# Kernel tuning notes

Measured on AMD Instinct MI355X. Metric: run time of the kernel, lower is better.

Reference implementation:

```python
import jax, jax.numpy as jnp
from jax import lax
import numpy as np

B, S, D, H = 16, 4096, 256, 256


def setup_inputs() -> dict:
    key = jax.random.key(0)
    k1, k2, k3, k4 = jax.random.split(key, 4)
    scale_x = 1.0 / np.sqrt(D)
    scale_h = 1.0 / np.sqrt(H)
    return {
        "inputs": jax.random.normal(k1, (B, S, D), dtype=jnp.float32),
        "state0": jnp.zeros((B, H), dtype=jnp.float32),
        "Wx": jax.random.normal(k2, (D, H), dtype=jnp.float32) * scale_x,
        "Wh": jax.random.normal(k3, (H, H), dtype=jnp.float32) * scale_h,
        "b": jnp.zeros((H,), dtype=jnp.float32),
    }


def reference(inputs, state0, Wx, Wh, b):
    # inputs: [B, S, D] -> time-major [S, B, D] (mirrors inputs.transpose_(0,1))
    x_tm = jnp.transpose(inputs, (1, 0, 2))
    # Precompute the input projection for all timesteps in one GEMM
    x_proj = jnp.einsum("sbd,dh->sbh", x_tm, Wx) + b  # [S, B, H]

    def step(h, xp_t):
        h_new = jnp.tanh(xp_t + h @ Wh)  # cell update; get_output = identity
        return h_new, h_new  # dropout p=0.0 -> identity

    _, outs = lax.scan(step, state0, x_proj)  # outs: [S, B, H]
    return jnp.transpose(outs, (1, 0, 2))  # back to [B, S, H]
```

## Files before the change

kernel.cpp:

```cpp
#include <hip/hip_runtime.h>

#define B_ 16
#define S_ 4096
#define D_ 256
#define H_ 256

typedef _Float16 h2 __attribute__((ext_vector_type(2)));
typedef _Float16 h8 __attribute__((ext_vector_type(8)));
typedef float f4 __attribute__((ext_vector_type(4)));

static __device__ __forceinline__ float fdot2f(h2 a, h2 b, float c) {
    return __builtin_amdgcn_fdot2(a, b, c, false);
}

template <int CTRL>
static __device__ __forceinline__ float dpp_qp(float v) {
    int r = __builtin_amdgcn_update_dpp(0, __float_as_int(v), CTRL, 0xF, 0xF, true);
    return __int_as_float(r);
}
#define DPP_XOR1 0xB1
#define DPP_XOR2 0x4E

static __device__ __forceinline__ int swz(int i) {
    const int s = i >> 6, r = (i >> 3) & 7, e = i & 7;
    return 64 * s + 8 * ((r + 2 * s) & 7) + e;
}

__global__ __launch_bounds__(256) void xproj_kernel(
    const float* __restrict__ x, const float* __restrict__ Wx,
    const float* __restrict__ bias, float* __restrict__ out)
{
    __shared__ float xs[32 * 256];
    const int tid = threadIdx.x;
    const long long row0 = (long long)blockIdx.x * 32;

    {
        const f4* __restrict__ xg = (const f4*)(x + row0 * D_);
        f4* xsv = (f4*)xs;
        #pragma unroll
        for (int k = 0; k < 8; ++k)
            xsv[tid + k * 256] = xg[tid + k * 256];
    }
    __syncthreads();

    const int j = tid;
    float acc[32];
    const float bj = bias[j];
    #pragma unroll
    for (int r = 0; r < 32; ++r) acc[r] = bj;

    for (int d4 = 0; d4 < D_ / 4; ++d4) {
        const float w0 = Wx[(d4 * 4 + 0) * H_ + j];
        const float w1 = Wx[(d4 * 4 + 1) * H_ + j];
        const float w2 = Wx[(d4 * 4 + 2) * H_ + j];
        const float w3 = Wx[(d4 * 4 + 3) * H_ + j];
        #pragma unroll
        for (int r = 0; r < 32; ++r) {
            f4 xv = *(const f4*)&xs[r * 256 + d4 * 4];
            acc[r] = fmaf(xv.x, w0, acc[r]);
            acc[r] = fmaf(xv.y, w1, acc[r]);
            acc[r] = fmaf(xv.z, w2, acc[r]);
            acc[r] = fmaf(xv.w, w3, acc[r]);
        }
    }
    #pragma unroll
    for (int r = 0; r < 32; ++r)
        out[(row0 + r) * H_ + j] = acc[r];
}

__global__ __launch_bounds__(256, 1) void scan_kernel(
    const float* __restrict__ Wh, const float* __restrict__ state0,
    float* __restrict__ out)
{
    __shared__ __align__(16) _Float16 hbuf[2][H_];
    const int tid = threadIdx.x;
    const int s = tid & 3;
    const int q = tid >> 2;
    const int b = blockIdx.x;
    const bool o1 = (s & 1) != 0;
    const bool o2 = (s & 2) != 0;

    h2 w[4][32];
    #pragma unroll
    for (int jj = 0; jj < 4; ++jj) {
        const int j = 4 * q + jj;
        #pragma unroll
        for (int ii = 0; ii < 32; ++ii) {
            const int i = 64 * s + 2 * ii;
            h2 p;
            p[0] = (_Float16)Wh[(long long)i * H_ + j];
            p[1] = (_Float16)Wh[(long long)(i + 1) * H_ + j];
            w[jj][ii] = p;
        }
    }

    hbuf[0][swz(tid)] = (_Float16)state0[b * H_ + tid];

    float* __restrict__ outb = out + (long long)b * S_ * H_;

    float xr[4];
    #pragma unroll
    for (int k = 0; k < 4; ++k)
        xr[k] = outb[(long long)k * H_ + tid];
    __syncthreads();

    #pragma unroll 4
    for (int st = 0; st < S_; ++st) {
        const int p = st & 1;
        const _Float16* hb = hbuf[p];

        h8 hv[8];
        #pragma unroll
        for (int r = 0; r < 8; ++r)
            hv[r] = *(const h8*)&hb[64 * s + 8 * ((r + 2 * s) & 7)];

        float acc0 = 0.f, acc1 = 0.f, acc2 = 0.f, acc3 = 0.f;
        #pragma unroll
        for (int r = 0; r < 8; ++r) {
            union { h8 v; h2 pr[4]; } u;
            u.v = hv[r];
            #pragma unroll
            for (int m = 0; m < 4; ++m) {
                const int ii = 4 * r + m;
                acc0 = fdot2f(u.pr[m], w[0][ii], acc0);
                acc1 = fdot2f(u.pr[m], w[1][ii], acc1);
                acc2 = fdot2f(u.pr[m], w[2][ii], acc2);
                acc3 = fdot2f(u.pr[m], w[3][ii], acc3);
            }
        }

        float vA = o1 ? acc1 : acc0;
        float vB = o1 ? acc3 : acc2;
        float sA = o1 ? acc0 : acc1;
        float sB = o1 ? acc2 : acc3;
        vA += dpp_qp<DPP_XOR1>(sA);
        vB += dpp_qp<DPP_XOR1>(sB);
        float v   = o2 ? vB : vA;
        float snd = o2 ? vA : vB;
        v += dpp_qp<DPP_XOR2>(snd);

        const float pre = v + xr[st & 3];
        const float e = __builtin_amdgcn_exp2f(pre * 2.8853900817779268f);
        const float hn = fmaf(-2.f, __builtin_amdgcn_rcpf(e + 1.f), 1.f);

        outb[(long long)st * H_ + tid] = hn;
        hbuf[p ^ 1][swz(tid)] = (_Float16)hn;

        const int nt = st + 4;
        xr[st & 3] = (nt < S_) ? outb[(long long)nt * H_ + tid] : 0.f;
        __syncthreads();
    }
}

extern "C" void kernel_launch(void* const* d_in, const int* in_sizes, int n_in,
                              void* d_out, int out_size, void* d_ws, size_t ws_size,
                              hipStream_t stream) {
    const float* x  = (const float*)d_in[0];
    const float* s0 = (const float*)d_in[1];
    const float* Wx = (const float*)d_in[2];
    const float* Wh = (const float*)d_in[3];
    const float* bv = (const float*)d_in[4];
    float* out = (float*)d_out;

    xproj_kernel<<<dim3((B_ * S_) / 32), dim3(256), 0, stream>>>(x, Wx, bv, out);
    scan_kernel<<<dim3(B_), dim3(256), 0, stream>>>(Wh, s0, out);
}
```

Before: 1.872 ms.

## Spread scan recurrence over 1024 threads, one output column per quad

The per-batch scan block grows from 256 to 1024 threads. Each quad of lanes now computes a single hidden column instead of four, which cuts the dot-product chain per thread by four and lets the reduction use a plain butterfly. Only lane 0 of each quad writes the output and the shared state. The cost is a barrier across 16 waves every timestep instead of 4, and three quarters of the lanes sit idle in the epilogue.

```diff
diff --git a/kernel.cpp b/kernel.cpp
--- a/kernel.cpp
+++ b/kernel.cpp
@@ -68,40 +68,37 @@
         out[(row0 + r) * H_ + j] = acc[r];
 }
 
-__global__ __launch_bounds__(256, 1) void scan_kernel(
+__global__ __launch_bounds__(1024, 1) void scan_kernel(
     const float* __restrict__ Wh, const float* __restrict__ state0,
     float* __restrict__ out)
 {
     __shared__ __align__(16) _Float16 hbuf[2][H_];
     const int tid = threadIdx.x;
     const int s = tid & 3;
-    const int q = tid >> 2;
+    const int j = tid >> 2;
     const int b = blockIdx.x;
-    const bool o1 = (s & 1) != 0;
-    const bool o2 = (s & 2) != 0;
+    const bool owner = (s == 0);
 
-    h2 w[4][32];
+    h2 w[32];
     #pragma unroll
-    for (int jj = 0; jj < 4; ++jj) {
-        const int j = 4 * q + jj;
-        #pragma unroll
-        for (int ii = 0; ii < 32; ++ii) {
-            const int i = 64 * s + 2 * ii;
-            h2 p;
-            p[0] = (_Float16)Wh[(long long)i * H_ + j];
-            p[1] = (_Float16)Wh[(long long)(i + 1) * H_ + j];
-            w[jj][ii] = p;
-        }
+    for (int ii = 0; ii < 32; ++ii) {
+        const int i = 64 * s + 2 * ii;
+        h2 p;
+        p[0] = (_Float16)Wh[(long long)i * H_ + j];
+        p[1] = (_Float16)Wh[(long long)(i + 1) * H_ + j];
+        w[ii] = p;
     }
 
-    hbuf[0][swz(tid)] = (_Float16)state0[b * H_ + tid];
+    if (owner) hbuf[0][swz(j)] = (_Float16)state0[b * H_ + j];
 
     float* __restrict__ outb = out + (long long)b * S_ * H_;
 
-    float xr[4];
-    #pragma unroll
-    for (int k = 0; k < 4; ++k)
-        xr[k] = outb[(long long)k * H_ + tid];
+    float xr[4] = {0.f, 0.f, 0.f, 0.f};
+    if (owner) {
+        #pragma unroll
+        for (int k = 0; k < 4; ++k)
+            xr[k] = outb[(long long)k * H_ + j];
+    }
     __syncthreads();
 
     #pragma unroll 4
@@ -114,40 +111,30 @@
         for (int r = 0; r < 8; ++r)
             hv[r] = *(const h8*)&hb[64 * s + 8 * ((r + 2 * s) & 7)];
 
-        float acc0 = 0.f, acc1 = 0.f, acc2 = 0.f, acc3 = 0.f;
+        float a0 = 0.f, a1 = 0.f, a2 = 0.f, a3 = 0.f;
         #pragma unroll
         for (int r = 0; r < 8; ++r) {
             union { h8 v; h2 pr[4]; } u;
             u.v = hv[r];
-            #pragma unroll
-            for (int m = 0; m < 4; ++m) {
-                const int ii = 4 * r + m;
-                acc0 = fdot2f(u.pr[m], w[0][ii], acc0);
-                acc1 = fdot2f(u.pr[m], w[1][ii], acc1);
-                acc2 = fdot2f(u.pr[m], w[2][ii], acc2);
-                acc3 = fdot2f(u.pr[m], w[3][ii], acc3);
-            }
+            a0 = fdot2f(u.pr[0], w[4 * r + 0], a0);
+            a1 = fdot2f(u.pr[1], w[4 * r + 1], a1);
+            a2 = fdot2f(u.pr[2], w[4 * r + 2], a2);
+            a3 = fdot2f(u.pr[3], w[4 * r + 3], a3);
         }
-
-        float vA = o1 ? acc1 : acc0;
-        float vB = o1 ? acc3 : acc2;
-        float sA = o1 ? acc0 : acc1;
-        float sB = o1 ? acc2 : acc3;
-        vA += dpp_qp<DPP_XOR1>(sA);
-        vB += dpp_qp<DPP_XOR1>(sB);
-        float v   = o2 ? vB : vA;
-        float snd = o2 ? vA : vB;
-        v += dpp_qp<DPP_XOR2>(snd);
+        float v = (a0 + a2) + (a1 + a3);
+        v += dpp_qp<DPP_XOR1>(v);
+        v += dpp_qp<DPP_XOR2>(v);
 
         const float pre = v + xr[st & 3];
         const float e = __builtin_amdgcn_exp2f(pre * 2.8853900817779268f);
         const float hn = fmaf(-2.f, __builtin_amdgcn_rcpf(e + 1.f), 1.f);
 
-        outb[(long long)st * H_ + tid] = hn;
-        hbuf[p ^ 1][swz(tid)] = (_Float16)hn;
-
-        const int nt = st + 4;
-        xr[st & 3] = (nt < S_) ? outb[(long long)nt * H_ + tid] : 0.f;
+        if (owner) {
+            outb[(long long)st * H_ + j] = hn;
+            hbuf[p ^ 1][swz(j)] = (_Float16)hn;
+            const int nt = st + 4;
+            xr[st & 3] = (nt < S_) ? outb[(long long)nt * H_ + j] : 0.f;
+        }
         __syncthreads();
     }
 }
@@ -163,5 +150,5 @@
     float* out = (float*)d_out;
 
     xproj_kernel<<<dim3((B_ * S_) / 32), dim3(256), 0, stream>>>(x, Wx, bv, out);
-    scan_kernel<<<dim3(B_), dim3(256), 0, stream>>>(Wh, s0, out);
+    scan_kernel<<<dim3(B_), dim3(1024), 0, stream>>>(Wh, s0, out);
 }
```

After: 2.357 ms. +25.9%, slower.
